# Kernel optimization log

Measured on AMD Instinct MI355X. Metric: run time of the kernel, lower is better.

## Reference

```python
import jax, jax.numpy as jnp
import numpy as np

NUM_ITERATIONS = 5
NUM_TERMS = 3  # (degree + 1) // 2 with degree = 5
INITIAL_SCALE = 1.1


def setup_inputs() -> dict:
    key = jax.random.key(0)
    k1, k2 = jax.random.split(key)
    X = jax.random.normal(k1, (64, 1024, 1024), dtype=jnp.float32)
    coefficients = jnp.array([3.4445, -4.7750, 2.0315], dtype=jnp.float32)
    return {"X": X, "coefficients": coefficients}


def reference(X, coefficients):
    # Normalize each matrix to Frobenius norm INITIAL_SCALE
    fro = jnp.sqrt(jnp.sum(X * X, axis=(-2, -1), keepdims=True))
    X = X / fro * INITIAL_SCALE
    for _ in range(NUM_ITERATIONS):
        # XTX = X^T X, shape [B, M, M]
        XTX = jnp.einsum('bji,bjk->bik', X, X)
        term = X
        acc = coefficients[0] * X
        for i in range(1, NUM_TERMS):
            term = jnp.einsum('bij,bjk->bik', term, XTX)  # X (X^T X)^i
            acc = acc + coefficients[i] * term
        X = acc
    return X
```

## Files before the change

kernel.cpp:

```cpp
#include <hip/hip_runtime.h>
#include <hip/hip_bf16.h>
#include <stdint.h>

typedef float f32x4 __attribute__((ext_vector_type(4)));
typedef short bf16x8 __attribute__((ext_vector_type(8)));

#define LDW 1024
#define BATCH_SH 20

__device__ __forceinline__ float b2f(__hip_bfloat16 h) { return __bfloat162float(h); }
__device__ __forceinline__ __hip_bfloat16 f2b(float f) { return __float2bfloat16(f); }

__global__ void k_partial(const float* __restrict__ xin, float* __restrict__ partials) {
  const int b = blockIdx.y, ch = blockIdx.x, t = threadIdx.x;
  const size_t base = ((size_t)b << BATCH_SH) + (size_t)ch * 16384;
  float s = 0.f;
#pragma unroll
  for (int i = 0; i < 16; ++i) {
    f32x4 v = *reinterpret_cast<const f32x4*>(xin + base + (size_t)(i * 256 + t) * 4);
    s += v[0] * v[0] + v[1] * v[1] + v[2] * v[2] + v[3] * v[3];
  }
#pragma unroll
  for (int off = 32; off; off >>= 1) s += __shfl_down(s, off);
  __shared__ float red[4];
  if ((t & 63) == 0) red[t >> 6] = s;
  __syncthreads();
  if (t == 0) partials[b * 64 + ch] = red[0] + red[1] + red[2] + red[3];
}

__global__ void k_scale(const float* __restrict__ partials, float* __restrict__ scales) {
  const int b = blockIdx.x, t = threadIdx.x;
  float s = partials[b * 64 + t];
#pragma unroll
  for (int off = 32; off; off >>= 1) s += __shfl_down(s, off);
  if (t == 0) scales[b] = 1.1f / sqrtf(s);
}

__global__ void k_scalesplit(const float* __restrict__ xin, const float* __restrict__ scales,
                             __hip_bfloat16* __restrict__ Xh, __hip_bfloat16* __restrict__ Xl,
                             __hip_bfloat16* __restrict__ XTh, __hip_bfloat16* __restrict__ XTl) {
  __shared__ float tile[64][65];
  const int b = blockIdx.z, tm = blockIdx.y, tn = blockIdx.x;
  const size_t boff = (size_t)b << BATCH_SH;
  const float s = scales[b];
  const int t = threadIdx.x, lr0 = t >> 6, lc = t & 63;
#pragma unroll
  for (int p = 0; p < 16; ++p) {
    const int lr = p * 4 + lr0;
    const size_t idx = boff + (size_t)(tm * 64 + lr) * LDW + tn * 64 + lc;
    const float v = xin[idx] * s;
    __hip_bfloat16 h = f2b(v);
    Xh[idx] = h;
    Xl[idx] = f2b(v - b2f(h));
    tile[lr][lc] = v;
  }
  __syncthreads();
#pragma unroll
  for (int p = 0; p < 16; ++p) {
    const int lr = p * 4 + lr0;
    const float v = tile[lc][lr];
    const size_t idx = boff + (size_t)(tn * 64 + lr) * LDW + tm * 64 + lc;
    __hip_bfloat16 h = f2b(v);
    XTh[idx] = h;
    XTl[idx] = f2b(v - b2f(h));
  }
}


#define SEGPTRS(S)                                                                        \
  const int seg_ = (S) >> 4, k0_ = ((S) & 15) << 6;                                       \
  const __hip_bfloat16* pa_ = seg_ == 0 ? pa0 : seg_ == 1 ? pa1 : pa2;                    \
  const __hip_bfloat16* pb_ = seg_ == 0 ? pb0 : seg_ == 1 ? pb1 : pb2;

#define LOAD_SLICE(S, P)                                                                  \
  {                                                                                       \
    SEGPTRS(S)                                                                            \
    const int r_ = (P) * 64 + srow;                                                       \
    sa[P] = *reinterpret_cast<const bf16x8*>(pa_ + boff + (size_t)(rowA + r_) * LDW +     \
                                             k0_ + chnk * 8);                             \
    sb[P] = *reinterpret_cast<const bf16x8*>(pb_ + boff + (size_t)(rowB + r_) * LDW +     \
                                             k0_ + chnk * 8);                             \
  }

#define DSW_SLICE(DB, P)                                                                  \
  {                                                                                       \
    char* wb_ = smem + (DB) * 65536;                                                      \
    const int r_ = (P) * 64 + srow;                                                       \
    const int sl_ = (chnk ^ (r_ & 7)) << 4;                                               \
    *reinterpret_cast<bf16x8*>(wb_ + r_ * 128 + sl_) = sa[P];                             \
    *reinterpret_cast<bf16x8*>(wb_ + 32768 + r_ * 128 + sl_) = sb[P];                     \
  }

#define DSREAD_AV(KK, MH)                                                                 \
  _Pragma("unroll") for (int i_ = 0; i_ < 4; ++i_)                                        \
      av[i_] = *reinterpret_cast<const bf16x8*>(smem + base + offA[KK][(MH) * 4 + i_]);

#define DSREAD_BV(KK)                                                                     \
  _Pragma("unroll") for (int i_ = 0; i_ < 4; ++i_)                                        \
      bv[i_] = *reinterpret_cast<const bf16x8*>(smem + base + offB[KK][i_]);

#define MFMA16(MH)                                                                        \
  __builtin_amdgcn_s_setprio(1);                                                          \
  _Pragma("unroll") for (int mi_ = 0; mi_ < 4; ++mi_)                                     \
      _Pragma("unroll") for (int ni_ = 0; ni_ < 4; ++ni_)                                 \
          acc[(MH) * 4 + mi_][ni_] = __builtin_amdgcn_mfma_f32_16x16x32_bf16(             \
              av[mi_], bv[ni_], acc[(MH) * 4 + mi_][ni_], 0, 0, 0);                       \
  __builtin_amdgcn_s_setprio(0);

#define BAR() __builtin_amdgcn_s_barrier()
#define LGKM0()                                       \
  asm volatile("s_waitcnt lgkmcnt(0)" ::: "memory"); \
  __builtin_amdgcn_sched_barrier(0)

#define PHASE(KK, MH, P)                                                                  \
  {                                                                                       \
    if ((MH) == 0) { DSREAD_BV(KK); }                                                     \
    DSREAD_AV(KK, MH);                                                                    \
    if (wr_ok) DSW_SLICE(wdb, P);                                                         \
    if (ld_ok) LOAD_SLICE(s + 2, P);                                                      \
    BAR();                                                                                \
    LGKM0();                                                                              \
    MFMA16(MH);                                                                           \
    BAR();                                                                                \
  }

template <int MODE>
__global__ __launch_bounds__(512, 2) void k_gemm(
    const __hip_bfloat16* __restrict__ pa0, const __hip_bfloat16* __restrict__ pa1,
    const __hip_bfloat16* __restrict__ pa2, const __hip_bfloat16* __restrict__ pb0,
    const __hip_bfloat16* __restrict__ pb1, const __hip_bfloat16* __restrict__ pb2,
    __hip_bfloat16* oh, __hip_bfloat16* ol,
    __hip_bfloat16* oth, __hip_bfloat16* otl,
    float* __restrict__ of,
    const __hip_bfloat16* __restrict__ eh, const __hip_bfloat16* __restrict__ el,
    const float* __restrict__ coef) {
  __shared__ __align__(16) char smem[131072];
  const int t = threadIdx.x;
  const int w = t >> 6, l = t & 63;
  const int wr = w >> 2, wc = w & 3;
  const int srow = t >> 3, chnk = t & 7;

  const int nwg = gridDim.x, q = nwg >> 3, r8 = nwg & 7;
  const int xcd = blockIdx.x & 7, o = blockIdx.x >> 3;
  const int wgid = (xcd < r8 ? xcd * (q + 1) : r8 * (q + 1) + (xcd - r8) * q) + o;

  int bat, tm, tn;
  if constexpr (MODE == 3) {
    bat = wgid >> 4;
    const int tile = wgid & 15;
    tm = tile >> 2; tn = tile & 3;
  } else {
    bat = (int)((unsigned)wgid / 10u);
    const int tile = wgid - bat * 10;
    tm = (tile < 4) ? 0 : (tile < 7) ? 1 : (tile < 9) ? 2 : 3;
    tn = (tile < 4) ? tile : (tile < 7) ? (tile - 3) : (tile < 9) ? (tile - 5) : 3;
  }
  const size_t boff = (size_t)bat << BATCH_SH;
  const int rowA = tm * 256, rowB = tn * 256;

  f32x4 acc[8][4];
#pragma unroll
  for (int i = 0; i < 8; ++i)
#pragma unroll
    for (int j = 0; j < 4; ++j) acc[i][j] = (f32x4){0.f, 0.f, 0.f, 0.f};

  int offA[2][8], offB[2][4];
#pragma unroll
  for (int kk = 0; kk < 2; ++kk) {
    const int g = kk * 4 + (l >> 4);
#pragma unroll
    for (int mi = 0; mi < 8; ++mi) {
      const int rA = wr * 128 + mi * 16 + (l & 15);
      offA[kk][mi] = rA * 128 + ((g ^ (rA & 7)) << 4);
    }
#pragma unroll
    for (int ni = 0; ni < 4; ++ni) {
      const int rB = wc * 64 + ni * 16 + (l & 15);
      offB[kk][ni] = 32768 + rB * 128 + ((g ^ (rB & 7)) << 4);
    }
  }

  bf16x8 sa[4], sb[4];
#pragma unroll
  for (int p = 0; p < 4; ++p) LOAD_SLICE(0, p);
#pragma unroll
  for (int p = 0; p < 4; ++p) DSW_SLICE(0, p);
#pragma unroll
  for (int p = 0; p < 4; ++p) LOAD_SLICE(1, p);
  LGKM0();
  BAR();

  for (int s = 0; s < 48; ++s) {
    const int base = (s & 1) * 65536;
    const int wdb = (s & 1) ^ 1;
    const bool wr_ok = (s + 1 < 48);
    const bool ld_ok = (s + 2 < 48);
    bf16x8 av[4], bv[4];
    PHASE(0, 0, 0)
    PHASE(0, 1, 1)
    PHASE(1, 0, 2)
    PHASE(1, 1, 3)
  }

  float c0 = 0.f, c1 = 0.f, c2 = 0.f;
  if constexpr (MODE == 2) { c0 = coef[0]; c1 = coef[1]; c2 = coef[2]; }
  const int r0 = tm * 256 + wr * 128 + ((l >> 4) << 2);
  const int cb = tn * 256 + wc * 64 + (l & 15);
#pragma unroll
  for (int mi = 0; mi < 8; ++mi) {
#pragma unroll
    for (int ni = 0; ni < 4; ++ni) {
      const int ccol = cb + ni * 16;
#pragma unroll
      for (int j = 0; j < 4; ++j) {
        const int rrow = r0 + mi * 16 + j;
        const size_t idx = boff + (size_t)rrow * LDW + ccol;
        const size_t tix = boff + (size_t)ccol * LDW + rrow;
        float v = acc[mi][ni][j];
        if constexpr (MODE == 2)
          v = c2 * v + c1 * (b2f(eh[idx]) + b2f(el[idx])) + (rrow == ccol ? c0 : 0.f);
        __hip_bfloat16 h = f2b(v);
        __hip_bfloat16 lo = f2b(v - b2f(h));
        if constexpr (MODE == 3) {
          if (oh) {
            oh[idx] = h; ol[idx] = lo;
            oth[tix] = h; otl[tix] = lo;
          }
          if (of) of[idx] = v;
        } else {
          oh[idx] = h; ol[idx] = lo;
          if (tm != tn) { oth[tix] = h; otl[tix] = lo; }
        }
      }
    }
  }
}

extern "C" void kernel_launch(void* const* d_in, const int* in_sizes, int n_in,
                              void* d_out, int out_size, void* d_ws, size_t ws_size,
                              hipStream_t stream) {
  (void)in_sizes; (void)n_in; (void)out_size;
  const float* xin = (const float*)d_in[0];
  const float* coef = (const float*)d_in[1];
  float* xout = (float*)d_out;

  int CH = 64;
  while (CH > 1 && ((size_t)CH * 16u * 1024u * 1024u + 65536u) > ws_size) CH >>= 1;

  const size_t nE = (size_t)CH << BATCH_SH;
  __hip_bfloat16* P0h = (__hip_bfloat16*)d_ws;
  __hip_bfloat16* P0l = P0h + nE;
  __hip_bfloat16* P1h = P0l + nE;
  __hip_bfloat16* P1l = P1h + nE;
  __hip_bfloat16* P2h = P1l + nE;
  __hip_bfloat16* P2l = P2h + nE;
  __hip_bfloat16* XTh = P2l + nE;
  __hip_bfloat16* XTl = XTh + nE;
  float* partials = (float*)(XTl + nE);
  float* scales = partials + (size_t)CH * 64;

  for (int c = 0; c < 64; c += CH) {
    const float* xi = xin + ((size_t)c << BATCH_SH);
    float* X = xout + ((size_t)c << BATCH_SH);
    k_partial<<<dim3(64, CH), 256, 0, stream>>>(xi, partials);
    k_scale<<<dim3(CH), 64, 0, stream>>>(partials, scales);
    k_scalesplit<<<dim3(16, 16, CH), 256, 0, stream>>>(xi, scales, P0h, P0l, XTh, XTl);

    __hip_bfloat16 *Xh = P0h, *Xl = P0l, *Ah = P1h, *Al = P1l, *Bh = P2h, *Bl = P2l;
    for (int it = 0; it < 5; ++it) {
      k_gemm<1><<<dim3(CH * 10), 512, 0, stream>>>(XTh, XTh, XTl, XTh, XTl, XTh,
                                                   Ah, Al, Ah, Al, nullptr,
                                                   nullptr, nullptr, nullptr);
      k_gemm<2><<<dim3(CH * 10), 512, 0, stream>>>(Ah, Ah, Al, Ah, Al, Ah,
                                                   Bh, Bl, Bh, Bl, nullptr,
                                                   Ah, Al, coef);
      k_gemm<3><<<dim3(CH * 16), 512, 0, stream>>>(Xh, Xh, Xl, Bh, Bl, Bh,
                                                   (it < 4) ? Ah : nullptr,
                                                   (it < 4) ? Al : nullptr,
                                                   XTh, XTl,
                                                   (it == 4) ? X : nullptr,
                                                   nullptr, nullptr, nullptr);
      __hip_bfloat16 *th = Xh, *tl = Xl;
      Xh = Ah; Xl = Al;
      Ah = Bh; Al = Bl;
      Bh = th; Bl = tl;
    }
  }
}
```

Before: 8.337 ms.

## Stage GEMM tiles via direct global-to-LDS loads instead of register round-trip

```diff
diff --git a/kernel.cpp b/kernel.cpp
--- a/kernel.cpp
+++ b/kernel.cpp
@@ -10,6 +10,12 @@
 
 __device__ __forceinline__ float b2f(__hip_bfloat16 h) { return __bfloat162float(h); }
 __device__ __forceinline__ __hip_bfloat16 f2b(float f) { return __float2bfloat16(f); }
+
+__device__ __forceinline__ void gload16(const void* g, void* l) {
+  __builtin_amdgcn_global_load_lds((const __attribute__((address_space(1))) void*)g,
+                                   (__attribute__((address_space(3))) void*)l,
+                                   16, 0, 0);
+}
 
 __global__ void k_partial(const float* __restrict__ xin, float* __restrict__ partials) {
   const int b = blockIdx.y, ch = blockIdx.x, t = threadIdx.x;
@@ -72,23 +78,16 @@
   const __hip_bfloat16* pa_ = seg_ == 0 ? pa0 : seg_ == 1 ? pa1 : pa2;                    \
   const __hip_bfloat16* pb_ = seg_ == 0 ? pb0 : seg_ == 1 ? pb1 : pb2;
 
-#define LOAD_SLICE(S, P)                                                                  \
+#define STAGE_SLICE(DB, S, P)                                                             \
   {                                                                                       \
     SEGPTRS(S)                                                                            \
-    const int r_ = (P) * 64 + srow;                                                       \
-    sa[P] = *reinterpret_cast<const bf16x8*>(pa_ + boff + (size_t)(rowA + r_) * LDW +     \
-                                             k0_ + chnk * 8);                             \
-    sb[P] = *reinterpret_cast<const bf16x8*>(pb_ + boff + (size_t)(rowB + r_) * LDW +     \
-                                             k0_ + chnk * 8);                             \
-  }
-
-#define DSW_SLICE(DB, P)                                                                  \
-  {                                                                                       \
-    char* wb_ = smem + (DB) * 65536;                                                      \
-    const int r_ = (P) * 64 + srow;                                                       \
-    const int sl_ = (chnk ^ (r_ & 7)) << 4;                                               \
-    *reinterpret_cast<bf16x8*>(wb_ + r_ * 128 + sl_) = sa[P];                             \
-    *reinterpret_cast<bf16x8*>(wb_ + 32768 + r_ * 128 + sl_) = sb[P];                     \
+    char* lb_ = smem + (DB) * 65536;                                                      \
+    const int r_ = (P) * 64 + w * 8 + (l >> 3);                                           \
+    const int kx_ = k0_ + (((l & 7) ^ (l >> 3)) << 3);                                    \
+    gload16(pa_ + boff + (size_t)(rowA + r_) * LDW + kx_,                                 \
+            lb_ + ((P) * 64 + w * 8) * 128 + l * 16);                                     \
+    gload16(pb_ + boff + (size_t)(rowB + r_) * LDW + kx_,                                 \
+            lb_ + 32768 + ((P) * 64 + w * 8) * 128 + l * 16);                             \
   }
 
 #define DSREAD_AV(KK, MH)                                                                 \
@@ -108,21 +107,10 @@
   __builtin_amdgcn_s_setprio(0);
 
 #define BAR() __builtin_amdgcn_s_barrier()
-#define LGKM0()                                       \
-  asm volatile("s_waitcnt lgkmcnt(0)" ::: "memory"); \
-  __builtin_amdgcn_sched_barrier(0)
-
-#define PHASE(KK, MH, P)                                                                  \
-  {                                                                                       \
-    if ((MH) == 0) { DSREAD_BV(KK); }                                                     \
-    DSREAD_AV(KK, MH);                                                                    \
-    if (wr_ok) DSW_SLICE(wdb, P);                                                         \
-    if (ld_ok) LOAD_SLICE(s + 2, P);                                                      \
-    BAR();                                                                                \
-    LGKM0();                                                                              \
-    MFMA16(MH);                                                                           \
-    BAR();                                                                                \
-  }
+#define SCB() __builtin_amdgcn_sched_barrier(0)
+#define LGKM0()                                        \
+  asm volatile("s_waitcnt lgkmcnt(0)" ::: "memory");   \
+  SCB()
 
 template <int MODE>
 __global__ __launch_bounds__(512, 2) void k_gemm(
@@ -138,7 +126,6 @@
   const int t = threadIdx.x;
   const int w = t >> 6, l = t & 63;
   const int wr = w >> 2, wc = w & 3;
-  const int srow = t >> 3, chnk = t & 7;
 
   const int nwg = gridDim.x, q = nwg >> 3, r8 = nwg & 7;
   const int xcd = blockIdx.x & 7, o = blockIdx.x >> 3;
@@ -180,26 +167,34 @@
     }
   }
 
-  bf16x8 sa[4], sb[4];
-#pragma unroll
-  for (int p = 0; p < 4; ++p) LOAD_SLICE(0, p);
-#pragma unroll
-  for (int p = 0; p < 4; ++p) DSW_SLICE(0, p);
-#pragma unroll
-  for (int p = 0; p < 4; ++p) LOAD_SLICE(1, p);
-  LGKM0();
+#pragma unroll
+  for (int p = 0; p < 4; ++p) STAGE_SLICE(0, 0, p);
+  asm volatile("s_waitcnt vmcnt(0)" ::: "memory");
+  SCB();
   BAR();
+  SCB();
 
   for (int s = 0; s < 48; ++s) {
     const int base = (s & 1) * 65536;
     const int wdb = (s & 1) ^ 1;
-    const bool wr_ok = (s + 1 < 48);
-    const bool ld_ok = (s + 2 < 48);
+    const bool ld_ok = (s + 1 < 48);
     bf16x8 av[4], bv[4];
-    PHASE(0, 0, 0)
-    PHASE(0, 1, 1)
-    PHASE(1, 0, 2)
-    PHASE(1, 1, 3)
+    DSREAD_BV(0);
+    DSREAD_AV(0, 0);
+    if (ld_ok) { STAGE_SLICE(wdb, s + 1, 0); STAGE_SLICE(wdb, s + 1, 1); }
+    BAR(); LGKM0(); MFMA16(0); BAR();
+    DSREAD_AV(0, 1);
+    if (ld_ok) { STAGE_SLICE(wdb, s + 1, 2); STAGE_SLICE(wdb, s + 1, 3); }
+    BAR(); LGKM0(); MFMA16(1); BAR();
+    DSREAD_BV(1);
+    DSREAD_AV(1, 0);
+    BAR(); LGKM0(); MFMA16(0); BAR();
+    DSREAD_AV(1, 1);
+    BAR(); LGKM0(); MFMA16(1);
+    asm volatile("s_waitcnt vmcnt(0)" ::: "memory");
+    SCB();
+    BAR();
+    SCB();
   }
 
   float c0 = 0.f, c1 = 0.f, c2 = 0.f;
```

Result: faster. 8.135 ms (-2.4%).
